# Kernel optimization log

Measured on AMD Instinct MI355X. Metric: run time of the kernel, lower is better.

## Reference

```python
import jax, jax.numpy as jnp
import numpy as np

N = 100_000      # nodes
E = 1_600_000    # edges (avg degree 16)
EMB = 32         # embedding_n
VOCAB = 100_000  # nodes_feats_size


def setup_inputs() -> dict:
    key = jax.random.key(0)
    ks = jax.random.split(key, 12)
    s = 1.0 / np.sqrt(EMB)
    return dict(
        features=jax.random.randint(ks[0], (N,), 0, VOCAB),
        cars=jax.random.uniform(ks[1], (N, 1), dtype=jnp.float32),
        entered=jax.random.uniform(ks[2], (N, 1), dtype=jnp.float32),
        free=jax.random.randint(ks[3], (N, 1), 0, 2).astype(jnp.float32),
        src=jax.random.randint(ks[4], (E,), 0, N),
        dst=jax.random.randint(ks[5], (E,), 0, N),
        embed_table=jax.random.normal(ks[6], (VOCAB, EMB), jnp.float32),
        W2n=jax.random.normal(ks[7], (EMB + 1, 1), jnp.float32) * s,
        b2n=jnp.zeros((1,), jnp.float32),
        W2e=jax.random.normal(ks[8], (2 * EMB, EMB), jnp.float32) * s,
        b2e=jnp.zeros((EMB,), jnp.float32),
        W3=jax.random.normal(ks[9], (EMB + 3, 8), jnp.float32) * s,
        b3=jnp.zeros((8,), jnp.float32),
        W4=jax.random.normal(ks[10], (8, 1), jnp.float32) * s,
        b4=jnp.zeros((1,), jnp.float32),
    )


def reference(features, cars, entered, free, src, dst,
              embed_table, W2n, b2n, W2e, b2e, W3, b3, W4, b4):
    relu = jax.nn.relu
    # --- apply_nodes: PredictParkingModule ---
    emb = embed_table[features]                                   # [N, EMB]
    parked = jnp.concatenate([emb, cars], axis=1) @ W2n + b2n     # [N, 1]
    cars1 = relu(relu(parked) + cars)                             # updated 'cars'
    # --- apply_edges: PredictEdgeProbModule ---
    he = jnp.concatenate([emb[src], emb[dst]], axis=1) @ W2e + b2e          # [E, EMB]
    h = relu(jnp.concatenate([he, cars1[src], cars1[dst], entered[src]], axis=1) @ W3 + b3)
    h = h @ W4 + b4                                                          # [E, 1]
    selfloop = (features[src] == features[dst]).astype(jnp.float32)[:, None]  # [E, 1]
    enabled = (selfloop != free[src]).astype(jnp.float32)                     # [E, 1]
    logit = relu(h) * enabled                                                 # [E, 1]
    # --- group_apply_edges(group_by='src'): per-source softmax over edges ---
    l = logit[:, 0]
    m = jax.lax.stop_gradient(jax.ops.segment_max(l, src, num_segments=N))
    ex = jnp.exp(l - m[src])
    ssum = jax.ops.segment_sum(ex, src, num_segments=N)
    prob = (ex / ssum[src])[:, None]                              # [E, 1]
    # --- pull: flow_message_func + flow_reduce_func (sum over dst) ---
    c = cars1[src] * prob                                         # all moving
    o = c * (1.0 - selfloop)                                      # outer
    cars_out = jax.ops.segment_sum(c, dst, num_segments=N)        # [N, 1]
    entered_out = jax.ops.segment_sum(o, dst, num_segments=N)     # [N, 1]
    return cars_out, emb, entered_out
```

## Files before the change

### kernel.cpp

```cpp
#include <hip/hip_runtime.h>
#include <stdint.h>

typedef _Float16 f16x8 __attribute__((ext_vector_type(8)));

#define RBITS 9
#define RSZ   512
#define G     512
#define MAXB  256
#define CHMAX 3200
#define RMAX  13

__device__ __forceinline__ uint32_t scanExcl256(uint32_t v, uint32_t* wtot, int t)
{
    uint32_t x = v;
    #pragma unroll
    for (int d = 1; d < 64; d <<= 1) {
        uint32_t y = __shfl_up(x, d, 64);
        if ((t & 63) >= d) x += y;
    }
    int w = t >> 6;
    if ((t & 63) == 63) wtot[w] = x;
    __syncthreads();
    uint32_t pre = 0;
    #pragma unroll
    for (int k = 0; k < 4; ++k) pre += (k < w) ? wtot[k] : 0;
    return pre + x - v;
}

__global__ __launch_bounds__(256) void node_kernel(
    const int*   __restrict__ features,
    const float* __restrict__ cars,
    const float* __restrict__ entered,
    const float* __restrict__ free_,
    const float* __restrict__ embed_table,
    const float* __restrict__ W2n,
    const float* __restrict__ b2n,
    const float* __restrict__ W2e,
    const float* __restrict__ W3,
    float* __restrict__ emb_out,
    float* __restrict__ cars1,
    f16x8* __restrict__ Ah,
    f16x8* __restrict__ Bh,
    float* __restrict__ sfree,
    int N)
{
    __shared__ float Wa[256], Wb[256];
    {
        int t = threadIdx.x, k = t >> 3, j = t & 7;
        float a = 0.f, b = 0.f;
        #pragma unroll
        for (int m = 0; m < 32; ++m) {
            float w3 = W3[m * 8 + j];
            a += W2e[k * 32 + m]        * w3;
            b += W2e[(32 + k) * 32 + m] * w3;
        }
        Wa[t] = a;
        Wb[t] = b;
    }
    __syncthreads();

    int i = blockIdx.x * blockDim.x + threadIdx.x;
    if (i >= N) return;
    int f = features[i];
    const float4* erow = (const float4*)(embed_table + (size_t)f * 32);
    float4* orow = (float4*)(emb_out + (size_t)i * 32);
    float e[32];
    #pragma unroll
    for (int q = 0; q < 8; ++q) {
        float4 v = erow[q];
        orow[q] = v;
        e[4*q+0] = v.x; e[4*q+1] = v.y; e[4*q+2] = v.z; e[4*q+3] = v.w;
    }
    float parked = b2n[0];
    #pragma unroll
    for (int k = 0; k < 32; ++k) parked += e[k] * W2n[k];
    float c = cars[i];
    parked += c * W2n[32];
    float c1 = fmaxf(fmaxf(parked, 0.f) + c, 0.f);
    cars1[i] = c1;
    float fm = (float)f + 1.f;
    sfree[i] = (free_[i] > 0.5f) ? -fm : fm;

    float ent = entered[i];
    float a8[8], b8[8];
    #pragma unroll
    for (int j = 0; j < 8; ++j) {
        a8[j] = c1 * W3[32*8 + j] + ent * W3[34*8 + j];
        b8[j] = c1 * W3[33*8 + j];
    }
    #pragma unroll
    for (int k = 0; k < 32; ++k) {
        float x = e[k];
        #pragma unroll
        for (int j = 0; j < 8; ++j) {
            a8[j] += x * Wa[k*8 + j];
            b8[j] += x * Wb[k*8 + j];
        }
    }
    f16x8 av, bv;
    #pragma unroll
    for (int j = 0; j < 8; ++j) { av[j] = (_Float16)a8[j]; bv[j] = (_Float16)b8[j]; }
    Ah[i] = av;
    Bh[i] = bv;
}

__global__ __launch_bounds__(256) void count_kernel(
    const int* __restrict__ src, const int* __restrict__ dst,
    uint32_t* __restrict__ cntS, uint32_t* __restrict__ cntD, int E, int B)
{
    __shared__ uint32_t cS[MAXB], cD[MAXB];
    for (int i = threadIdx.x; i < MAXB; i += 256) { cS[i] = 0; cD[i] = 0; }
    __syncthreads();
    int per = (E + G - 1) / G;
    int lo = blockIdx.x * per, hi = min(E, lo + per);
    for (int i = lo + threadIdx.x; i < hi; i += 256) {
        atomicAdd(&cS[src[i] >> RBITS], 1u);
        atomicAdd(&cD[dst[i] >> RBITS], 1u);
    }
    __syncthreads();
    for (int i = threadIdx.x; i < B; i += 256) {
        cntS[(size_t)i * G + blockIdx.x] = cS[i];
        cntD[(size_t)i * G + blockIdx.x] = cD[i];
    }
}

__global__ __launch_bounds__(512) void scanA_kernel(
    uint32_t* __restrict__ cntS, uint32_t* __restrict__ cntD,
    uint32_t* __restrict__ totS, uint32_t* __restrict__ totD, int B)
{
    __shared__ uint32_t sh[G];
    int arr = (int)(blockIdx.x >= (unsigned)B);
    int b = blockIdx.x - (arr ? B : 0);
    uint32_t* a   = arr ? cntD : cntS;
    uint32_t* tot = arr ? totD : totS;
    int t = threadIdx.x;
    uint32_t v = a[(size_t)b * G + t];
    sh[t] = v;
    __syncthreads();
    for (int d = 1; d < G; d <<= 1) {
        uint32_t u = (t >= d) ? sh[t - d] : 0;
        __syncthreads();
        sh[t] += u;
        __syncthreads();
    }
    a[(size_t)b * G + t] = sh[t] - v;
    if (t == G - 1) tot[b] = sh[t];
}

__global__ __launch_bounds__(256) void scanB_kernel(
    const uint32_t* __restrict__ totS, const uint32_t* __restrict__ totD,
    uint32_t* __restrict__ baseS, uint32_t* __restrict__ baseD, int B)
{
    __shared__ uint32_t sh[256];
    int t = threadIdx.x;
    uint32_t v = (t < B) ? totS[t] : 0;
    sh[t] = v; __syncthreads();
    for (int d = 1; d < 256; d <<= 1) {
        uint32_t u = (t >= d) ? sh[t - d] : 0;
        __syncthreads(); sh[t] += u; __syncthreads();
    }
    if (t < B) baseS[t] = sh[t] - v;
    __syncthreads();
    uint32_t v2 = (t < B) ? totD[t] : 0;
    sh[t] = v2; __syncthreads();
    for (int d = 1; d < 256; d <<= 1) {
        uint32_t u = (t >= d) ? sh[t - d] : 0;
        __syncthreads(); sh[t] += u; __syncthreads();
    }
    if (t < B) baseD[t] = sh[t] - v2;
}

__global__ __launch_bounds__(256) void scatter_kernel(
    const int* __restrict__ src, const int* __restrict__ dst,
    const float* __restrict__ sfree,
    const f16x8* __restrict__ Ah, const f16x8* __restrict__ Bh,
    const float* __restrict__ b2e, const float* __restrict__ W3,
    const float* __restrict__ b3,  const float* __restrict__ W4,
    const float* __restrict__ b4,
    const uint32_t* __restrict__ cntS, const uint32_t* __restrict__ cntD,
    const uint32_t* __restrict__ baseS, const uint32_t* __restrict__ baseD,
    uint32_t* __restrict__ payloadS,
    uint32_t* __restrict__ DLa,
    uint16_t* __restrict__ DHa,
    int E, int B)
{
    __shared__ float b3p[8];
    __shared__ uint32_t curS[MAXB], curD[MAXB];
    __shared__ uint32_t tblS[MAXB], tblD[MAXB];
    __shared__ uint32_t wtot[4];
    __shared__ uint32_t buf[CHMAX];
    __shared__ uint16_t bid[CHMAX];

    int t = threadIdx.x, g = blockIdx.x;
    tblS[t] = 0; tblD[t] = 0;
    if (t < B) {
        curS[t] = baseS[t] + cntS[(size_t)t * G + g];
        curD[t] = baseD[t] + cntD[(size_t)t * G + g];
    }
    if (t < 8) {
        float s = b3[t];
        #pragma unroll
        for (int m = 0; m < 32; ++m) s += b2e[m] * W3[m * 8 + t];
        b3p[t] = s;
    }
    __syncthreads();
    float w4[8]; float bias4 = b4[0];
    #pragma unroll
    for (int j = 0; j < 8; ++j) w4[j] = W4[j];

    int per = (E + G - 1) / G;
    int lo = g * per, hi = min(E, lo + per), n = hi - lo;

    uint32_t regA[RMAX], regB[RMAX], regC[RMAX];
    #pragma unroll
    for (int r = 0; r < RMAX; ++r) {
        int idx = r * 256 + t;
        if (idx < n) {
            int i = lo + idx;
            int s = src[i], d = dst[i];
            f16x8 av = Ah[s], bv = Bh[d];
            float fsv = sfree[s];
            float fdv = sfree[d];
            float out = bias4;
            #pragma unroll
            for (int j = 0; j < 8; ++j)
                out += fmaxf((float)av[j] + (float)bv[j] + b3p[j], 0.f) * w4[j];
            bool self  = (fabsf(fsv) == fabsf(fdv));
            bool freeS = (fsv < 0.f);
            float l = (self != freeS) ? fmaxf(out, 0.f) : 0.f;
            float ex = __expf(l);
            uint32_t exb = (uint32_t)__builtin_bit_cast(unsigned short, (_Float16)ex);
            uint32_t keyS = (uint32_t)s >> RBITS;
            uint32_t keyD = (uint32_t)d >> RBITS;
            uint32_t rankS = atomicAdd(&tblS[keyS], 1u);
            uint32_t rankD = atomicAdd(&tblD[keyD], 1u);
            regA[r] = keyS | (rankS << 8) | (self ? 0x80000000u : 0u);
            regB[r] = keyD | (rankD << 8) | ((uint32_t)(d & (RSZ - 1)) << 21);
            regC[r] = (uint32_t)(s & (RSZ - 1)) | (exb << 16);
        }
    }
    __syncthreads();
    uint32_t vS = tblS[t], vD = tblD[t];
    __syncthreads();
    uint32_t eS = scanExcl256(vS, wtot, t);
    __syncthreads();
    uint32_t eD = scanExcl256(vD, wtot, t);
    tblS[t] = eS;
    tblD[t] = eD;
    __syncthreads();

    #pragma unroll
    for (int r = 0; r < RMAX; ++r) {
        int idx = r * 256 + t;
        if (idx < n) {
            uint32_t key = regA[r] & 255u;
            uint32_t slot = tblS[key] + ((regA[r] >> 8) & 0xFFFu);
            buf[slot] = regC[r];
            bid[slot] = (uint16_t)key;
        }
    }
    __syncthreads();
    for (int j = t; j < n; j += 256) {
        uint32_t b = bid[j];
        payloadS[curS[b] + (j - tblS[b])] = buf[j];
    }
    __syncthreads();

    #pragma unroll
    for (int r = 0; r < RMAX; ++r) {
        int idx = r * 256 + t;
        if (idx < n) {
            uint32_t key = regB[r] & 255u;
            uint32_t slot = tblD[key] + ((regB[r] >> 8) & 0xFFFu);
            uint32_t s = ((regA[r] & 255u) << RBITS) | (regC[r] & (RSZ - 1));
            buf[slot] = s | (((regB[r] >> 21) & 0x1FFu) << 17)
                      | (regA[r] & 0x80000000u);
            bid[slot] = (uint16_t)key;
        }
    }
    __syncthreads();
    for (int j = t; j < n; j += 256) {
        uint32_t b = bid[j];
        DLa[curD[b] + (j - tblD[b])] = buf[j];
    }
    __syncthreads();

    #pragma unroll
    for (int r = 0; r < RMAX; ++r) {
        int idx = r * 256 + t;
        if (idx < n) {
            uint32_t key = regB[r] & 255u;
            uint32_t slot = tblD[key] + ((regB[r] >> 8) & 0xFFFu);
            buf[slot] = regC[r] >> 16;
        }
    }
    __syncthreads();
    for (int j = t; j < n; j += 256) {
        uint32_t b = bid[j];
        DHa[curD[b] + (j - tblD[b])] = (uint16_t)buf[j];
    }
}

__global__ __launch_bounds__(256) void bucketS_kernel(
    const uint32_t* __restrict__ baseS, const uint32_t* __restrict__ payloadS,
    const float* __restrict__ cars1, float* __restrict__ ratio,
    int N, int B, int E)
{
    __shared__ float acc[RSZ];
    int b = blockIdx.x, t = threadIdx.x;
    for (int i = t; i < RSZ; i += 256) acc[i] = 0.f;
    __syncthreads();
    uint32_t beg = baseS[b];
    uint32_t end = (b == B - 1) ? (uint32_t)E : baseS[b + 1];
    for (uint32_t i = beg + t; i < end; i += 256) {
        uint32_t p = payloadS[i];
        float v = (float)__builtin_bit_cast(_Float16, (unsigned short)(p >> 16));
        atomicAdd(&acc[p & (RSZ - 1)], v);
    }
    __syncthreads();
    int nb = b << RBITS;
    for (int i = t; i < RSZ; i += 256) {
        int node = nb + i;
        if (node < N) {
            float s = acc[i];
            ratio[node] = cars1[node] / (s > 0.f ? s : 1.f);
        }
    }
}

__global__ __launch_bounds__(256) void bucketD_kernel(
    const uint32_t* __restrict__ baseD,
    const uint32_t* __restrict__ DLa, const uint16_t* __restrict__ DHa,
    const float* __restrict__ ratio,
    float* __restrict__ cars_out, float* __restrict__ entered_out,
    int N, int B, int E)
{
    __shared__ float accC[RSZ], accX[RSZ];
    int b = blockIdx.x, t = threadIdx.x;
    for (int i = t; i < RSZ; i += 256) { accC[i] = 0.f; accX[i] = 0.f; }
    __syncthreads();
    uint32_t beg = baseD[b];
    uint32_t end = (b == B - 1) ? (uint32_t)E : baseD[b + 1];
    for (uint32_t i = beg + t; i < end; i += 256) {
        uint32_t m = DLa[i];
        float ex = (float)__builtin_bit_cast(_Float16, (unsigned short)DHa[i]);
        int s  = m & 0x1FFFF;
        int ld = (m >> 17) & (RSZ - 1);
        float c = ratio[s] * ex;
        atomicAdd(&accC[ld], c);
        if (m & 0x80000000u) atomicAdd(&accX[ld], c);
    }
    __syncthreads();
    int nb = b << RBITS;
    for (int i = t; i < RSZ; i += 256) {
        int node = nb + i;
        if (node < N) {
            float cs = accC[i];
            cars_out[node]    = cs;
            entered_out[node] = cs - accX[i];
        }
    }
}

extern "C" void kernel_launch(void* const* d_in, const int* in_sizes, int n_in,
                              void* d_out, int out_size, void* d_ws, size_t ws_size,
                              hipStream_t stream)
{
    const int N = in_sizes[0];
    const int E = in_sizes[4];
    const int B = (N + RSZ - 1) / RSZ;
    const int L = B * G;

    const int*   features    = (const int*)  d_in[0];
    const float* cars        = (const float*)d_in[1];
    const float* entered     = (const float*)d_in[2];
    const float* free_       = (const float*)d_in[3];
    const int*   src         = (const int*)  d_in[4];
    const int*   dst         = (const int*)  d_in[5];
    const float* embed_table = (const float*)d_in[6];
    const float* W2n         = (const float*)d_in[7];
    const float* b2n         = (const float*)d_in[8];
    const float* W2e         = (const float*)d_in[9];
    const float* b2e         = (const float*)d_in[10];
    const float* W3          = (const float*)d_in[11];
    const float* b3          = (const float*)d_in[12];
    const float* W4          = (const float*)d_in[13];
    const float* b4          = (const float*)d_in[14];

    float* out         = (float*)d_out;
    float* cars_out    = out;
    float* emb_out     = out + N;
    float* entered_out = out + (size_t)N * 33;

    float*    ws       = (float*)d_ws;
    float*    cars1    = ws;
    float*    ratio    = ws + N;
    float*    sfree    = ws + (size_t)2 * N;
    f16x8*    Ah       = (f16x8*)(ws + (size_t)4 * N);
    f16x8*    Bh       = (f16x8*)(ws + (size_t)8 * N);
    uint32_t* cntS     = (uint32_t*)(ws + (size_t)12 * N);
    uint32_t* cntD     = cntS + L;
    uint32_t* totS     = cntD + L;
    uint32_t* totD     = totS + MAXB;
    uint32_t* baseS    = totD + MAXB;
    uint32_t* baseD    = baseS + MAXB;
    uint32_t* payloadS = baseD + MAXB;
    uint32_t* DLa      = payloadS + E;
    uint16_t* DHa      = (uint16_t*)(DLa + E);

    node_kernel<<<(N + 255) / 256, 256, 0, stream>>>(
        features, cars, entered, free_, embed_table, W2n, b2n, W2e, W3,
        emb_out, cars1, Ah, Bh, sfree, N);
    count_kernel<<<G, 256, 0, stream>>>(src, dst, cntS, cntD, E, B);
    scanA_kernel<<<2 * B, G, 0, stream>>>(cntS, cntD, totS, totD, B);
    scanB_kernel<<<1, 256, 0, stream>>>(totS, totD, baseS, baseD, B);
    scatter_kernel<<<G, 256, 0, stream>>>(
        src, dst, sfree, Ah, Bh, b2e, W3, b3, W4, b4,
        cntS, cntD, baseS, baseD, payloadS, DLa, DHa, E, B);
    bucketS_kernel<<<B, 256, 0, stream>>>(baseS, payloadS, cars1, ratio, N, B, E);
    bucketD_kernel<<<B, 256, 0, stream>>>(
        baseD, DLa, DHa, ratio, cars_out, entered_out, N, B, E);
}
```

Before: 103.3 us.

## Fuse node and count kernels, drop scanB, double edge chunk grid

The count pass is merged into the node kernel, giving a single launch over G=1024 blocks; blocks beyond N/256 only do counting. The separate bucket-base scan kernel is removed: each consumer (scatter, bucketS, bucketD) recomputes the exclusive scan of the per-bucket totals locally. The edge partition grid doubles to 1024 chunks with smaller per-thread register arrays and a smaller LDS staging buffer, and scanA is changed to handle two elements per thread. The aim is fewer kernel launches and more parallel scatter blocks, at the price of redundant scan work in every block and a larger count matrix to scan.

```diff
diff --git a/kernel.cpp b/kernel.cpp
--- a/kernel.cpp
+++ b/kernel.cpp
@@ -5,10 +5,10 @@
 
 #define RBITS 9
 #define RSZ   512
-#define G     512
+#define G     1024
 #define MAXB  256
-#define CHMAX 3200
-#define RMAX  13
+#define CHMAX 1568
+#define RMAX  7
 
 __device__ __forceinline__ uint32_t scanExcl256(uint32_t v, uint32_t* wtot, int t)
 {
@@ -27,7 +27,7 @@
     return pre + x - v;
 }
 
-__global__ __launch_bounds__(256) void node_kernel(
+__global__ __launch_bounds__(256) void nodecount_kernel(
     const int*   __restrict__ features,
     const float* __restrict__ cars,
     const float* __restrict__ entered,
@@ -37,16 +37,35 @@
     const float* __restrict__ b2n,
     const float* __restrict__ W2e,
     const float* __restrict__ W3,
+    const int* __restrict__ src, const int* __restrict__ dst,
     float* __restrict__ emb_out,
     float* __restrict__ cars1,
     f16x8* __restrict__ Ah,
     f16x8* __restrict__ Bh,
     float* __restrict__ sfree,
-    int N)
-{
+    uint32_t* __restrict__ cntS, uint32_t* __restrict__ cntD,
+    int N, int E, int B)
+{
+    __shared__ uint32_t cS[MAXB], cD[MAXB];
+    int t = threadIdx.x, g = blockIdx.x;
+    for (int i = t; i < MAXB; i += 256) { cS[i] = 0; cD[i] = 0; }
+    __syncthreads();
+    int per = (E + G - 1) / G;
+    int lo = g * per, hi = min(E, lo + per);
+    for (int i = lo + t; i < hi; i += 256) {
+        atomicAdd(&cS[src[i] >> RBITS], 1u);
+        atomicAdd(&cD[dst[i] >> RBITS], 1u);
+    }
+    __syncthreads();
+    for (int i = t; i < B; i += 256) {
+        cntS[(size_t)i * G + g] = cS[i];
+        cntD[(size_t)i * G + g] = cD[i];
+    }
+
+    if (g * 256 >= N) return;
     __shared__ float Wa[256], Wb[256];
     {
-        int t = threadIdx.x, k = t >> 3, j = t & 7;
+        int k = t >> 3, j = t & 7;
         float a = 0.f, b = 0.f;
         #pragma unroll
         for (int m = 0; m < 32; ++m) {
@@ -59,7 +78,7 @@
     }
     __syncthreads();
 
-    int i = blockIdx.x * blockDim.x + threadIdx.x;
+    int i = g * 256 + t;
     if (i >= N) return;
     int f = features[i];
     const float4* erow = (const float4*)(embed_table + (size_t)f * 32);
@@ -104,70 +123,31 @@
     Bh[i] = bv;
 }
 
-__global__ __launch_bounds__(256) void count_kernel(
-    const int* __restrict__ src, const int* __restrict__ dst,
-    uint32_t* __restrict__ cntS, uint32_t* __restrict__ cntD, int E, int B)
-{
-    __shared__ uint32_t cS[MAXB], cD[MAXB];
-    for (int i = threadIdx.x; i < MAXB; i += 256) { cS[i] = 0; cD[i] = 0; }
-    __syncthreads();
-    int per = (E + G - 1) / G;
-    int lo = blockIdx.x * per, hi = min(E, lo + per);
-    for (int i = lo + threadIdx.x; i < hi; i += 256) {
-        atomicAdd(&cS[src[i] >> RBITS], 1u);
-        atomicAdd(&cD[dst[i] >> RBITS], 1u);
-    }
-    __syncthreads();
-    for (int i = threadIdx.x; i < B; i += 256) {
-        cntS[(size_t)i * G + blockIdx.x] = cS[i];
-        cntD[(size_t)i * G + blockIdx.x] = cD[i];
-    }
-}
-
 __global__ __launch_bounds__(512) void scanA_kernel(
     uint32_t* __restrict__ cntS, uint32_t* __restrict__ cntD,
     uint32_t* __restrict__ totS, uint32_t* __restrict__ totD, int B)
 {
-    __shared__ uint32_t sh[G];
+    __shared__ uint32_t sh[512];
     int arr = (int)(blockIdx.x >= (unsigned)B);
     int b = blockIdx.x - (arr ? B : 0);
     uint32_t* a   = arr ? cntD : cntS;
     uint32_t* tot = arr ? totD : totS;
     int t = threadIdx.x;
-    uint32_t v = a[(size_t)b * G + t];
-    sh[t] = v;
-    __syncthreads();
-    for (int d = 1; d < G; d <<= 1) {
+    size_t base = (size_t)b * G + (size_t)t * 2;
+    uint32_t v0 = a[base], v1 = a[base + 1];
+    uint32_t p = v0 + v1;
+    sh[t] = p;
+    __syncthreads();
+    for (int d = 1; d < 512; d <<= 1) {
         uint32_t u = (t >= d) ? sh[t - d] : 0;
         __syncthreads();
         sh[t] += u;
         __syncthreads();
     }
-    a[(size_t)b * G + t] = sh[t] - v;
-    if (t == G - 1) tot[b] = sh[t];
-}
-
-__global__ __launch_bounds__(256) void scanB_kernel(
-    const uint32_t* __restrict__ totS, const uint32_t* __restrict__ totD,
-    uint32_t* __restrict__ baseS, uint32_t* __restrict__ baseD, int B)
-{
-    __shared__ uint32_t sh[256];
-    int t = threadIdx.x;
-    uint32_t v = (t < B) ? totS[t] : 0;
-    sh[t] = v; __syncthreads();
-    for (int d = 1; d < 256; d <<= 1) {
-        uint32_t u = (t >= d) ? sh[t - d] : 0;
-        __syncthreads(); sh[t] += u; __syncthreads();
-    }
-    if (t < B) baseS[t] = sh[t] - v;
-    __syncthreads();
-    uint32_t v2 = (t < B) ? totD[t] : 0;
-    sh[t] = v2; __syncthreads();
-    for (int d = 1; d < 256; d <<= 1) {
-        uint32_t u = (t >= d) ? sh[t - d] : 0;
-        __syncthreads(); sh[t] += u; __syncthreads();
-    }
-    if (t < B) baseD[t] = sh[t] - v2;
+    uint32_t exc = sh[t] - p;
+    a[base] = exc;
+    a[base + 1] = exc + v0;
+    if (t == 511) tot[b] = sh[t];
 }
 
 __global__ __launch_bounds__(256) void scatter_kernel(
@@ -178,7 +158,7 @@
     const float* __restrict__ b3,  const float* __restrict__ W4,
     const float* __restrict__ b4,
     const uint32_t* __restrict__ cntS, const uint32_t* __restrict__ cntD,
-    const uint32_t* __restrict__ baseS, const uint32_t* __restrict__ baseD,
+    const uint32_t* __restrict__ totS, const uint32_t* __restrict__ totD,
     uint32_t* __restrict__ payloadS,
     uint32_t* __restrict__ DLa,
     uint16_t* __restrict__ DHa,
@@ -192,11 +172,16 @@
     __shared__ uint16_t bid[CHMAX];
 
     int t = threadIdx.x, g = blockIdx.x;
+    uint32_t vS = (t < B) ? totS[t] : 0;
+    uint32_t eS = scanExcl256(vS, wtot, t);
+    __syncthreads();
+    uint32_t vD = (t < B) ? totD[t] : 0;
+    uint32_t eD = scanExcl256(vD, wtot, t);
+    if (t < B) {
+        curS[t] = eS + cntS[(size_t)t * G + g];
+        curD[t] = eD + cntD[(size_t)t * G + g];
+    }
     tblS[t] = 0; tblD[t] = 0;
-    if (t < B) {
-        curS[t] = baseS[t] + cntS[(size_t)t * G + g];
-        curD[t] = baseD[t] + cntD[(size_t)t * G + g];
-    }
     if (t < 8) {
         float s = b3[t];
         #pragma unroll
@@ -240,13 +225,13 @@
         }
     }
     __syncthreads();
-    uint32_t vS = tblS[t], vD = tblD[t];
-    __syncthreads();
-    uint32_t eS = scanExcl256(vS, wtot, t);
-    __syncthreads();
-    uint32_t eD = scanExcl256(vD, wtot, t);
-    tblS[t] = eS;
-    tblD[t] = eD;
+    uint32_t hS = tblS[t], hD = tblD[t];
+    __syncthreads();
+    uint32_t bS = scanExcl256(hS, wtot, t);
+    __syncthreads();
+    uint32_t bD = scanExcl256(hD, wtot, t);
+    tblS[t] = bS;
+    tblD[t] = bD;
     __syncthreads();
 
     #pragma unroll
@@ -254,7 +239,7 @@
         int idx = r * 256 + t;
         if (idx < n) {
             uint32_t key = regA[r] & 255u;
-            uint32_t slot = tblS[key] + ((regA[r] >> 8) & 0xFFFu);
+            uint32_t slot = tblS[key] + ((regA[r] >> 8) & 0x7FFu);
             buf[slot] = regC[r];
             bid[slot] = (uint16_t)key;
         }
@@ -271,7 +256,7 @@
         int idx = r * 256 + t;
         if (idx < n) {
             uint32_t key = regB[r] & 255u;
-            uint32_t slot = tblD[key] + ((regB[r] >> 8) & 0xFFFu);
+            uint32_t slot = tblD[key] + ((regB[r] >> 8) & 0x7FFu);
             uint32_t s = ((regA[r] & 255u) << RBITS) | (regC[r] & (RSZ - 1));
             buf[slot] = s | (((regB[r] >> 21) & 0x1FFu) << 17)
                       | (regA[r] & 0x80000000u);
@@ -290,7 +275,7 @@
         int idx = r * 256 + t;
         if (idx < n) {
             uint32_t key = regB[r] & 255u;
-            uint32_t slot = tblD[key] + ((regB[r] >> 8) & 0xFFFu);
+            uint32_t slot = tblD[key] + ((regB[r] >> 8) & 0x7FFu);
             buf[slot] = regC[r] >> 16;
         }
     }
@@ -302,20 +287,24 @@
 }
 
 __global__ __launch_bounds__(256) void bucketS_kernel(
-    const uint32_t* __restrict__ baseS, const uint32_t* __restrict__ payloadS,
+    const uint32_t* __restrict__ totS, const uint32_t* __restrict__ payloadS,
     const float* __restrict__ cars1, float* __restrict__ ratio,
-    int N, int B, int E)
+    int N, int B)
 {
     __shared__ float acc[RSZ];
+    __shared__ uint32_t wtot[4];
+    __shared__ uint32_t be[2];
     int b = blockIdx.x, t = threadIdx.x;
+    uint32_t v = (t < B) ? totS[t] : 0;
+    uint32_t e = scanExcl256(v, wtot, t);
+    if (t == b) { be[0] = e; be[1] = e + v; }
     for (int i = t; i < RSZ; i += 256) acc[i] = 0.f;
     __syncthreads();
-    uint32_t beg = baseS[b];
-    uint32_t end = (b == B - 1) ? (uint32_t)E : baseS[b + 1];
+    uint32_t beg = be[0], end = be[1];
     for (uint32_t i = beg + t; i < end; i += 256) {
         uint32_t p = payloadS[i];
-        float v = (float)__builtin_bit_cast(_Float16, (unsigned short)(p >> 16));
-        atomicAdd(&acc[p & (RSZ - 1)], v);
+        float val = (float)__builtin_bit_cast(_Float16, (unsigned short)(p >> 16));
+        atomicAdd(&acc[p & (RSZ - 1)], val);
     }
     __syncthreads();
     int nb = b << RBITS;
@@ -329,18 +318,22 @@
 }
 
 __global__ __launch_bounds__(256) void bucketD_kernel(
-    const uint32_t* __restrict__ baseD,
+    const uint32_t* __restrict__ totD,
     const uint32_t* __restrict__ DLa, const uint16_t* __restrict__ DHa,
     const float* __restrict__ ratio,
     float* __restrict__ cars_out, float* __restrict__ entered_out,
-    int N, int B, int E)
+    int N, int B)
 {
     __shared__ float accC[RSZ], accX[RSZ];
+    __shared__ uint32_t wtot[4];
+    __shared__ uint32_t be[2];
     int b = blockIdx.x, t = threadIdx.x;
+    uint32_t v = (t < B) ? totD[t] : 0;
+    uint32_t e = scanExcl256(v, wtot, t);
+    if (t == b) { be[0] = e; be[1] = e + v; }
     for (int i = t; i < RSZ; i += 256) { accC[i] = 0.f; accX[i] = 0.f; }
     __syncthreads();
-    uint32_t beg = baseD[b];
-    uint32_t end = (b == B - 1) ? (uint32_t)E : baseD[b + 1];
+    uint32_t beg = be[0], end = be[1];
     for (uint32_t i = beg + t; i < end; i += 256) {
         uint32_t m = DLa[i];
         float ex = (float)__builtin_bit_cast(_Float16, (unsigned short)DHa[i]);
@@ -402,22 +395,18 @@
     uint32_t* cntD     = cntS + L;
     uint32_t* totS     = cntD + L;
     uint32_t* totD     = totS + MAXB;
-    uint32_t* baseS    = totD + MAXB;
-    uint32_t* baseD    = baseS + MAXB;
-    uint32_t* payloadS = baseD + MAXB;
+    uint32_t* payloadS = totD + MAXB;
     uint32_t* DLa      = payloadS + E;
     uint16_t* DHa      = (uint16_t*)(DLa + E);
 
-    node_kernel<<<(N + 255) / 256, 256, 0, stream>>>(
+    nodecount_kernel<<<G, 256, 0, stream>>>(
         features, cars, entered, free_, embed_table, W2n, b2n, W2e, W3,
-        emb_out, cars1, Ah, Bh, sfree, N);
-    count_kernel<<<G, 256, 0, stream>>>(src, dst, cntS, cntD, E, B);
-    scanA_kernel<<<2 * B, G, 0, stream>>>(cntS, cntD, totS, totD, B);
-    scanB_kernel<<<1, 256, 0, stream>>>(totS, totD, baseS, baseD, B);
+        src, dst, emb_out, cars1, Ah, Bh, sfree, cntS, cntD, N, E, B);
+    scanA_kernel<<<2 * B, 512, 0, stream>>>(cntS, cntD, totS, totD, B);
     scatter_kernel<<<G, 256, 0, stream>>>(
         src, dst, sfree, Ah, Bh, b2e, W3, b3, W4, b4,
-        cntS, cntD, baseS, baseD, payloadS, DLa, DHa, E, B);
-    bucketS_kernel<<<B, 256, 0, stream>>>(baseS, payloadS, cars1, ratio, N, B, E);
+        cntS, cntD, totS, totD, payloadS, DLa, DHa, E, B);
+    bucketS_kernel<<<B, 256, 0, stream>>>(totS, payloadS, cars1, ratio, N, B);
     bucketD_kernel<<<B, 256, 0, stream>>>(
-        baseD, DLa, DHa, ratio, cars_out, entered_out, N, B, E);
-}
+        totD, DLa, DHa, ratio, cars_out, entered_out, N, B);
+}
```

New measurement: 100.2 us. -3.0%, faster.
